# Optimization experiments

Hardware: AMD Instinct MI355X
Metric: run time of the kernel (lower is better)

Reference implementation:

```python
import jax, jax.numpy as jnp
import numpy as np

DIM = 768  # N, feature length and Linear dim
B, C = 16, 1024  # batch, token count


def setup_inputs() -> dict:
    key = jax.random.key(0)
    ks = jax.random.split(key, 7)
    s = 1.0 / np.sqrt(DIM)
    return {
        "x": jax.random.normal(ks[0], (B, C, DIM), dtype=jnp.float32),
        "Wq": jax.random.uniform(ks[1], (DIM, DIM), jnp.float32, -s, s),
        "bq": jax.random.uniform(ks[2], (DIM,), jnp.float32, -s, s),
        "Wk": jax.random.uniform(ks[3], (DIM, DIM), jnp.float32, -s, s),
        "bk": jax.random.uniform(ks[4], (DIM,), jnp.float32, -s, s),
        "Wv": jax.random.uniform(ks[5], (DIM, DIM), jnp.float32, -s, s),
        "bv": jax.random.uniform(ks[6], (DIM,), jnp.float32, -s, s),
    }


def reference(x, Wq, bq, Wk, bk, Wv, bv):
    # x: [B, C, N] with N == DIM; Linears act on last axis (torch y = x W^T + b)
    Bb, Cc, N = x.shape
    q = jnp.einsum("bcn,dn->bcd", x, Wq) + bq
    k = jnp.einsum("bcn,dn->bcd", x, Wk) + bk
    v = jnp.einsum("bcn,dn->bcd", x, Wv) + bv
    attn = jax.nn.softmax(jnp.einsum("bcd,bed->bce", q, k) * (N ** -0.5), axis=-1)  # [B,C,C]
    out = jnp.einsum("bce,ben->bcn", attn, v)  # [B,C,N]
    # faithful to torch: transpose(1,2) then reshape back to (B,C,N) -- a buffer reinterpretation
    out = jnp.transpose(out, (0, 2, 1)).reshape(Bb, Cc, N)
    return out + x  # dropout is identity at inference
```

## Files before the change

### kernel.cpp

```cpp
#include <hip/hip_runtime.h>
#include <hip/hip_bf16.h>

typedef __bf16 v8bf __attribute__((ext_vector_type(8)));
typedef float f32x4 __attribute__((ext_vector_type(4)));

static __device__ __forceinline__ unsigned short f2b(float f){
  union { float f; unsigned int u; } c; c.f = f;
  return (unsigned short)((c.u + 0x7FFFu + ((c.u >> 16) & 1u)) >> 16);
}
static __device__ __forceinline__ float b2f(unsigned int h){
  union { unsigned int u; float f; } c; c.u = h << 16; return c.f;
}

static __device__ __forceinline__ void gld_lds16(const void* g, void* l){
  __builtin_amdgcn_global_load_lds(
      (const __attribute__((address_space(1))) unsigned int*)g,
      (__attribute__((address_space(3))) unsigned int*)l, 16, 0, 0);
}

#define FENCE __builtin_amdgcn_sched_barrier(0)

static __device__ __forceinline__ void gemm128(
    const unsigned short* __restrict__ A, int lda,
    const unsigned short* __restrict__ B, int ldb,
    int NT, unsigned short* smem, f32x4 acc[4][3])
{
  const int tid  = threadIdx.x;
  const int lane = tid & 63;
  const int w    = tid >> 6;
  const int wr   = w >> 2, wc = w & 3;
  const int lr   = lane & 15, lg = lane >> 4;
  char* sm = (char*)smem;

  #pragma unroll
  for (int m=0;m<4;++m)
    #pragma unroll
    for (int n=0;n<3;++n)
      acc[m][n] = (f32x4){0.f,0.f,0.f,0.f};

  const int rloc = tid >> 3;
  const int scol = ((tid & 7) ^ ((tid >> 3) & 7)) << 3;
  const unsigned short* Ab0 = A + (size_t)rloc*lda + scol;
  const unsigned short* Bb0 = B + (size_t)rloc*ldb + scol;

  auto stA = [&](int d, int i, int kE){
    gld_lds16(Ab0 + (size_t)(i*64)*lda + kE, sm + d*16384 + i*8192 + w*1024);
  };
  auto stB = [&](int d, int i, int kE){
    gld_lds16(Bb0 + (size_t)(i*64)*ldb + kE, sm + 32768 + d*24576 + i*8192 + w*1024);
  };

  const int ce0 = (((lg*8))      ^ ((lr&7)<<3)) * 2;
  const int ce1 = (((32 + lg*8)) ^ ((lr&7)<<3)) * 2;

  stA(0,0,0); stA(0,1,0);
  stB(0,0,0); stB(0,1,0); stB(0,2,0);
  asm volatile("s_waitcnt vmcnt(0)" ::: "memory");
  __builtin_amdgcn_s_barrier();

  for (int kt = 0; kt < NT; ++kt) {
    const int d  = kt & 1;
    const int kN = (kt+1 < NT ? kt+1 : NT-1)*64;
    stA(d^1,0,kN); stA(d^1,1,kN);
    stB(d^1,0,kN); stB(d^1,1,kN); stB(d^1,2,kN);
    v8bf a[4][2], b[3][2];
    char* Abase = sm + d*16384;
    char* Bbase = sm + 32768 + d*24576;
    #pragma unroll
    for (int m=0;m<4;++m){
      char* rp = Abase + (wr*64 + m*16 + lr)*128;
      a[m][0] = *(const v8bf*)(rp + ce0);
      a[m][1] = *(const v8bf*)(rp + ce1);
    }
    #pragma unroll
    for (int n=0;n<3;++n){
      char* rp = Bbase + (wc*48 + n*16 + lr)*128;
      b[n][0] = *(const v8bf*)(rp + ce0);
      b[n][1] = *(const v8bf*)(rp + ce1);
    }
    FENCE; asm volatile("s_waitcnt lgkmcnt(0)" ::: "memory"); FENCE;
    __builtin_amdgcn_s_setprio(1);
    #pragma unroll
    for (int m=0;m<4;++m)
      #pragma unroll
      for (int n=0;n<3;++n){
        acc[m][n] = __builtin_amdgcn_mfma_f32_16x16x32_bf16(a[m][0], b[n][0], acc[m][n], 0,0,0);
        acc[m][n] = __builtin_amdgcn_mfma_f32_16x16x32_bf16(a[m][1], b[n][1], acc[m][n], 0,0,0);
      }
    __builtin_amdgcn_s_setprio(0);
    asm volatile("s_waitcnt vmcnt(0)" ::: "memory");
    __builtin_amdgcn_s_barrier();
  }
}

template<int NW, bool DEEP>
static __device__ __forceinline__ void gemmcore(
    const unsigned short* __restrict__ A, int lda,
    const unsigned short* __restrict__ B, int ldb,
    int NT, unsigned short* smem, f32x4 acc[8][NW])
{
  const int tid  = threadIdx.x;
  const int lane = tid & 63;
  const int w    = tid >> 6;
  const int wr   = w >> 2, wc = w & 3;
  const int lr   = lane & 15, lg = lane >> 4;
  char* sm = (char*)smem;
  constexpr int NAB   = DEEP ? 3 : 2;
  constexpr int BBASE = NAB * 32768;
  constexpr int BBUF  = NW * 8192;

  #pragma unroll
  for (int m=0;m<8;++m)
    #pragma unroll
    for (int n=0;n<NW;++n)
      acc[m][n] = (f32x4){0.f,0.f,0.f,0.f};

  const int rloc = tid >> 3;
  const int scol = ((tid & 7) ^ ((tid >> 3) & 7)) << 3;
  const unsigned short* Ab0 = A + (size_t)rloc*lda + scol;
  const unsigned short* Bb0 = B + (size_t)rloc*ldb + scol;

  auto stA = [&](int ab, int i, int kE){
    gld_lds16(Ab0 + (size_t)(i*64)*lda + kE, sm + ab*32768 + i*8192 + w*1024);
  };
  auto stB = [&](int db, int i, int kE){
    gld_lds16(Bb0 + (size_t)(i*64)*ldb + kE, sm + BBASE + db*BBUF + i*8192 + w*1024);
  };

  const int ce0 = (((lg*8))      ^ ((lr&7)<<3)) * 2;
  const int ce1 = (((32 + lg*8)) ^ ((lr&7)<<3)) * 2;

  v8bf bX[NW][2], bY[NW][2], af0[2][2], af1[2][2];

  auto rdA = [&](v8bf (&dst)[2][2], char* base, int qq){
    #pragma unroll
    for (int mm=0;mm<2;++mm){
      char* rp = base + ((qq*2+mm)*16+lr)*128;
      dst[mm][0] = *(const v8bf*)(rp + ce0);
      dst[mm][1] = *(const v8bf*)(rp + ce1);
    }
  };
  auto rdB = [&](v8bf (&dst)[NW][2], char* base){
    #pragma unroll
    for (int n=0;n<NW;++n){
      char* rp = base + (n*16+lr)*128;
      dst[n][0] = *(const v8bf*)(rp + ce0);
      dst[n][1] = *(const v8bf*)(rp + ce1);
    }
  };
  auto domfma = [&](v8bf (&a)[2][2], v8bf (&bb)[NW][2], int qq){
    __builtin_amdgcn_s_setprio(1);
    #pragma unroll
    for (int mm=0;mm<2;++mm)
      #pragma unroll
      for (int n=0;n<NW;++n){
        acc[qq*2+mm][n] = __builtin_amdgcn_mfma_f32_16x16x32_bf16(a[mm][0], bb[n][0], acc[qq*2+mm][n], 0,0,0);
        acc[qq*2+mm][n] = __builtin_amdgcn_mfma_f32_16x16x32_bf16(a[mm][1], bb[n][1], acc[qq*2+mm][n], 0,0,0);
      }
    __builtin_amdgcn_s_setprio(0);
  };

  auto ktile = [&](int kt, int ar, int an, int as,
                   v8bf (&bc)[NW][2], v8bf (&bn)[NW][2]){
    char* Ab = sm + ar*32768 + wr*16384;
    char* An = sm + an*32768 + wr*16384;
    char* Bn = sm + BBASE + ((kt+1)&1)*BBUF + wc*(NW*2048);
    const int kAraw = DEEP ? kt+2 : kt+1;
    const int kA = (kAraw < NT ? kAraw : NT-1)*64;
    const int kB = (kt+2 < NT ? kt+2 : NT-1)*64;
    const int db = kt & 1;

    stA(as,0,kA); stA(as,1,kA);
    rdA(af1, Ab, 1);
    FENCE; asm volatile("s_waitcnt lgkmcnt(4)" ::: "memory"); FENCE;
    domfma(af0, bc, 0);
    __builtin_amdgcn_s_barrier();

    stA(as,2,kA); stA(as,3,kA);
    rdA(af0, Ab, 2);
    FENCE; asm volatile("s_waitcnt lgkmcnt(4)" ::: "memory"); FENCE;
    domfma(af1, bc, 1);
    __builtin_amdgcn_s_barrier();

    stB(db,0,kB); stB(db,1,kB);
    rdA(af1, Ab, 3);
    FENCE; asm volatile("s_waitcnt lgkmcnt(4)" ::: "memory"); FENCE;
    domfma(af0, bc, 2);
    if constexpr (DEEP) asm volatile("s_waitcnt vmcnt(6)" ::: "memory");
    else                asm volatile("s_waitcnt vmcnt(2)" ::: "memory");
    __builtin_amdgcn_s_barrier();

    #pragma unroll
    for (int i=2;i<NW;++i) stB(db,i,kB);
    rdA(af0, An, 0);
    rdB(bn, Bn);
    if constexpr (NW==3) { FENCE; asm volatile("s_waitcnt lgkmcnt(10)" ::: "memory"); FENCE; }
    else                 { FENCE; asm volatile("s_waitcnt lgkmcnt(12)" ::: "memory"); FENCE; }
    domfma(af1, bc, 3);
    __builtin_amdgcn_s_barrier();
  };

  #pragma unroll
  for (int i=0;i<4;++i)  stA(0,i,0);
  #pragma unroll
  for (int i=0;i<NW;++i) stB(0,i,0);
  if constexpr (DEEP) {
    #pragma unroll
    for (int i=0;i<4;++i) stA(1,i,64);
  }
  #pragma unroll
  for (int i=0;i<NW;++i) stB(1,i,64);
  if constexpr (DEEP)      asm volatile("s_waitcnt vmcnt(7)" ::: "memory");
  else if constexpr (NW==3) asm volatile("s_waitcnt vmcnt(3)" ::: "memory");
  else                      asm volatile("s_waitcnt vmcnt(4)" ::: "memory");
  __builtin_amdgcn_s_barrier();
  rdB(bX, sm + BBASE + wc*(NW*2048));
  rdA(af0, sm + wr*16384, 0);

  if constexpr (DEEP) {
    int c0 = 0;
    for (int kt = 0; kt < NT; kt += 2) {
      const int c1 = (c0+1==3) ? 0 : c0+1;
      const int c2 = (c1+1==3) ? 0 : c1+1;
      ktile(kt,   c0, c1, c2, bX, bY);
      ktile(kt+1, c1, c2, c0, bY, bX);
      c0 = c2;
    }
  } else {
    for (int kt = 0; kt < NT; kt += 2) {
      ktile(kt,   0, 1, 1, bX, bY);
      ktile(kt+1, 1, 0, 0, bY, bX);
    }
  }
}

__global__ __launch_bounds__(256) void convert_kernel(
    const float* __restrict__ x,
    const float* __restrict__ Wq, const float* __restrict__ Wk,
    const float* __restrict__ Wv,
    unsigned short* __restrict__ Xb, unsigned short* __restrict__ Wb)
{
  const int NX = 3145728;
  const int NW_ = 147456;
  const int total = NX + 3*NW_;
  for (int i = blockIdx.x*256 + threadIdx.x; i < total; i += gridDim.x*256) {
    const float* src; unsigned short* dst; int off;
    if (i < NX) { src = x; dst = Xb; off = i; }
    else {
      int j = i - NX; int z = j / NW_; off = j - z*NW_;
      src = (z==0) ? Wq : ((z==1) ? Wk : Wv);
      dst = Wb + (size_t)z*589824;
    }
    float4 v = reinterpret_cast<const float4*>(src)[off];
    ushort4 h; h.x=f2b(v.x); h.y=f2b(v.y); h.z=f2b(v.z); h.w=f2b(v.w);
    reinterpret_cast<ushort4*>(dst)[off] = h;
  }
}

__global__ __launch_bounds__(512, 4) void qkv_kernel(
    const unsigned short* __restrict__ Xb, const unsigned short* __restrict__ Wb,
    const float* __restrict__ bq, const float* __restrict__ bk,
    const float* __restrict__ bv,
    unsigned short* __restrict__ Qb, unsigned short* __restrict__ Kb,
    unsigned short* __restrict__ Vt)
{
  extern __shared__ unsigned short smem[];
  const int bid = blockIdx.x;
  const int wg  = (bid & 7)*192 + (bid >> 3);
  const int mt  = wg / 12, nt = wg % 12;

  f32x4 acc[4][3];
  gemm128(Xb + (size_t)mt*128*768, 768,
          Wb + (size_t)nt*192*768, 768, 12, smem, acc);

  const int tid = threadIdx.x, lane = tid & 63, w = tid >> 6;
  const int wr = w >> 2, wc = w & 3, lr = lane & 15, lg = lane >> 4;
  const int z = nt >> 2;
  const float* bias = (z==0) ? bq : ((z==1) ? bk : bv);
  const int colbase = (nt & 3)*192 + wc*48;

  if (z < 2) {
    unsigned short* dst = (z==0) ? Qb : Kb;
    #pragma unroll
    for (int m=0;m<4;++m){
      int row0 = mt*128 + wr*64 + m*16 + lg*4;
      #pragma unroll
      for (int n=0;n<3;++n){
        int col = colbase + n*16 + lr;
        float bb = bias[col];
        #pragma unroll
        for (int r=0;r<4;++r)
          dst[(size_t)(row0+r)*768 + col] = f2b(acc[m][n][r] + bb);
      }
    }
  } else {
    const int batch = mt >> 3;
    const int ebase = (mt & 7)*128;
    unsigned short* dst = Vt + (size_t)batch*786432;
    #pragma unroll
    for (int m=0;m<4;++m){
      int e0 = ebase + wr*64 + m*16 + lg*4;
      #pragma unroll
      for (int n=0;n<3;++n){
        int col = colbase + n*16 + lr;
        float bb = bias[col];
        ushort4 h;
        h.x = f2b(acc[m][n][0] + bb);
        h.y = f2b(acc[m][n][1] + bb);
        h.z = f2b(acc[m][n][2] + bb);
        h.w = f2b(acc[m][n][3] + bb);
        *reinterpret_cast<ushort4*>(dst + (size_t)col*1024 + e0) = h;
      }
    }
  }
}

__global__ __launch_bounds__(512, 2) void scores_kernel(
    const unsigned short* __restrict__ Qb,
    const unsigned short* __restrict__ Kb,
    unsigned short* __restrict__ Eb)
{
  extern __shared__ unsigned short smem[];
  const int lid = blockIdx.x;
  const int seq = lid >> 3;
  const int b   = (lid & 7)*2 + (seq >> 4);
  const int t   = seq & 15;
  const int mt  = t >> 2, nt = t & 3;

  f32x4 acc[8][4];
  gemmcore<4,false>(Qb + (size_t)b*786432 + (size_t)mt*256*768, 768,
                    Kb + (size_t)b*786432 + (size_t)nt*256*768, 768,
                    12, smem, acc);

  const float scale = 0.03608439182435161f;
  const int tid = threadIdx.x, lane = tid & 63, w = tid >> 6;
  const int wr = w >> 2, wc = w & 3, lr = lane & 15, lg = lane >> 4;
  unsigned short* dst = Eb + (size_t)b*1048576;
  #pragma unroll
  for (int m=0;m<8;++m){
    int row0 = mt*256 + wr*128 + m*16 + lg*4;
    #pragma unroll
    for (int n=0;n<4;++n){
      int col = nt*256 + wc*64 + n*16 + lr;
      #pragma unroll
      for (int r=0;r<4;++r)
        dst[(size_t)(row0+r)*1024 + col] = f2b(__expf(acc[m][n][r] * scale));
    }
  }
}

__global__ __launch_bounds__(256) void rowsum_kernel(
    const unsigned short* __restrict__ E, float* __restrict__ D)
{
  int row  = blockIdx.x*4 + (threadIdx.x >> 6);
  int lane = threadIdx.x & 63;
  const unsigned short* p = E + (size_t)row*1024 + lane*16;
  uint4 v0 = *reinterpret_cast<const uint4*>(p);
  uint4 v1 = *reinterpret_cast<const uint4*>(p + 8);
  unsigned int uu[8] = {v0.x, v0.y, v0.z, v0.w, v1.x, v1.y, v1.z, v1.w};
  float s = 0.f;
  #pragma unroll
  for (int i=0;i<8;++i){ s += b2f(uu[i] & 0xffffu); s += b2f(uu[i] >> 16); }
  #pragma unroll
  for (int off=1; off<64; off<<=1) s += __shfl_xor(s, off, 64);
  if (lane == 0) D[row] = s;
}

__global__ __launch_bounds__(512, 2) void pv_kernel(
    const unsigned short* __restrict__ Eb,
    const unsigned short* __restrict__ Vt,
    const float* __restrict__ D,
    const float* __restrict__ x, float* __restrict__ out)
{
  extern __shared__ unsigned short smem[];
  const int lid = blockIdx.x;
  const int seq = lid >> 3;
  const int b   = (lid & 7)*2 + (seq >> 4);
  const int t   = seq & 15;
  const int mt  = t >> 2, nt = t & 3;

  f32x4 acc[8][3];
  gemmcore<3,true>(Eb + (size_t)b*1048576 + (size_t)mt*256*1024, 1024,
                   Vt + (size_t)b*786432  + (size_t)nt*192*1024, 1024,
                   16, smem, acc);

  const int tid = threadIdx.x, lane = tid & 63, w = tid >> 6;
  const int wr = w >> 2, wc = w & 3, lr = lane & 15, lg = lane >> 4;
  const float* xb = x   + (size_t)b*786432;
  float*       ob = out + (size_t)b*786432;
  const float* Db = D + b*1024;
  #pragma unroll
  for (int m=0;m<8;++m){
    int c0 = mt*256 + wr*128 + m*16 + lg*4;
    float inv0 = 1.0f / Db[c0+0];
    float inv1 = 1.0f / Db[c0+1];
    float inv2 = 1.0f / Db[c0+2];
    float inv3 = 1.0f / Db[c0+3];
    #pragma unroll
    for (int n=0;n<3;++n){
      int col = nt*192 + wc*48 + n*16 + lr;
      size_t idx = (size_t)col*1024 + c0;
      float4 xv = *reinterpret_cast<const float4*>(xb + idx);
      float4 o;
      o.x = acc[m][n][0]*inv0 + xv.x;
      o.y = acc[m][n][1]*inv1 + xv.y;
      o.z = acc[m][n][2]*inv2 + xv.z;
      o.w = acc[m][n][3]*inv3 + xv.w;
      *reinterpret_cast<float4*>(ob + idx) = o;
    }
  }
}

extern "C" void kernel_launch(void* const* d_in, const int* in_sizes, int n_in,
                              void* d_out, int out_size, void* d_ws, size_t ws_size,
                              hipStream_t stream)
{
  const float* x  = (const float*)d_in[0];
  const float* Wq = (const float*)d_in[1];
  const float* bq = (const float*)d_in[2];
  const float* Wk = (const float*)d_in[3];
  const float* bk = (const float*)d_in[4];
  const float* Wv = (const float*)d_in[5];
  const float* bv = (const float*)d_in[6];
  float* out = (float*)d_out;

  char* ws = (char*)d_ws;
  unsigned short* Xb = (unsigned short*)(ws);
  unsigned short* Wb = (unsigned short*)(ws + 25165824);
  unsigned short* Eb = (unsigned short*)(ws);
  unsigned short* Qb = (unsigned short*)(ws + 33554432);
  float*          Dd = (float*)         (ws + 33554432);
  unsigned short* Kb = (unsigned short*)(ws + 58720256);
  unsigned short* Vt = (unsigned short*)(ws + 83886080);

  convert_kernel<<<dim3(2048), dim3(256), 0,      stream>>>(x, Wq, Wk, Wv, Xb, Wb);
  qkv_kernel    <<<dim3(1536), dim3(512), 81920,  stream>>>(Xb, Wb, bq, bk, bv, Qb, Kb, Vt);
  scores_kernel <<<dim3(256),  dim3(512), 131072, stream>>>(Qb, Kb, Eb);
  rowsum_kernel <<<dim3(4096), dim3(256), 0,      stream>>>(Eb, Dd);
  pv_kernel     <<<dim3(256),  dim3(512), 147456, stream>>>(Eb, Vt, Dd, x, out);
}
```

Measured before the change: 144.4 us.

## Replace scores GEMM core with 8-phase, triple-buffered-B pipelined schedule

Adds a new GEMM core (gemm8p) for the QK^T scores kernel. It splits each K tile into four quadrant phases, interleaving global-to-LDS loads with MFMA work, and triple-buffers the B operand. The pv kernel keeps the old deep schedule, now specialised into gemmpv without templates. Scores LDS grows to 160KB, which could limit occupancy, and the extra barriers per phase add sync overhead.

```diff
diff --git a/kernel.cpp b/kernel.cpp
--- a/kernel.cpp
+++ b/kernel.cpp
@@ -19,6 +19,105 @@
 }
 
 #define FENCE __builtin_amdgcn_sched_barrier(0)
+
+static __device__ __forceinline__ void gemm8p(
+    const unsigned short* __restrict__ A, int lda,
+    const unsigned short* __restrict__ B, int ldb,
+    int NT, unsigned short* smem, f32x4 acc[8][4])
+{
+  const int tid  = threadIdx.x;
+  const int lane = tid & 63;
+  const int w    = tid >> 6;
+  const int wr   = w >> 2, wc = w & 3;
+  const int lr   = lane & 15, lg = lane >> 4;
+  char* sm = (char*)smem;
+
+  #pragma unroll
+  for (int m=0;m<8;++m)
+    #pragma unroll
+    for (int n=0;n<4;++n)
+      acc[m][n] = (f32x4){0.f,0.f,0.f,0.f};
+
+  const int rloc = tid >> 3;
+  const int scol = ((tid & 7) ^ ((tid >> 3) & 7)) << 3;
+  const unsigned short* Ab0 = A + (size_t)rloc*lda + scol;
+  const unsigned short* Bb0 = B + (size_t)rloc*ldb + scol;
+
+  auto stA2 = [&](int slot, int h, int kE){
+    gld_lds16(Ab0 + (size_t)(h*128)*lda + kE,      sm + slot*32768 + h*16384 + w*1024);
+    gld_lds16(Ab0 + (size_t)(h*128+64)*lda + kE,   sm + slot*32768 + h*16384 + 8192 + w*1024);
+  };
+  auto stB2 = [&](int slot, int h, int kE){
+    gld_lds16(Bb0 + (size_t)(h*128)*ldb + kE,      sm + 65536 + slot*32768 + h*16384 + w*1024);
+    gld_lds16(Bb0 + (size_t)(h*128+64)*ldb + kE,   sm + 65536 + slot*32768 + h*16384 + 8192 + w*1024);
+  };
+
+  const int ce0 = (((lg*8))      ^ ((lr&7)<<3)) * 2;
+  const int ce1 = (((32 + lg*8)) ^ ((lr&7)<<3)) * 2;
+
+  stA2(0,0,0); stA2(0,1,0);
+  stB2(0,0,0); stB2(0,1,0);
+  stB2(1,0,64); stB2(1,1,64);
+  asm volatile("s_waitcnt vmcnt(4)" ::: "memory");
+  __builtin_amdgcn_s_barrier();
+
+  int b0 = 0;
+  for (int kt = 0; kt < NT; kt += 2) {
+    const int b1 = (b0+1==3)?0:b0+1;
+    const int b2 = (b1+1==3)?0:b1+1;
+    const int kA1 = (kt+1 < NT ? kt+1 : NT-1)*64;
+    const int k2  = (kt+2 < NT ? kt+2 : NT-1)*64;
+    const int k3  = (kt+3 < NT ? kt+3 : NT-1)*64;
+
+    #pragma unroll
+    for (int tp=0; tp<2; ++tp) {
+      const int rdB = (tp==0) ? b0 : b1;
+      #pragma unroll
+      for (int q=0; q<4; ++q) {
+        const int mh = q>>1, nh = q&1;
+        v8bf a[4][2], b[2][2];
+        char* Ab = sm + tp*32768;
+        #pragma unroll
+        for (int mm=0;mm<4;++mm){
+          char* rp = Ab + (wr*128 + mh*64 + mm*16 + lr)*128;
+          a[mm][0] = *(const v8bf*)(rp + ce0);
+          a[mm][1] = *(const v8bf*)(rp + ce1);
+        }
+        char* Bb = sm + 65536 + rdB*32768;
+        #pragma unroll
+        for (int nn=0;nn<2;++nn){
+          char* rp = Bb + (wc*64 + nh*32 + nn*16 + lr)*128;
+          b[nn][0] = *(const v8bf*)(rp + ce0);
+          b[nn][1] = *(const v8bf*)(rp + ce1);
+        }
+        if      (tp==0 && q==0) stA2(1, 0, kA1);
+        else if (tp==0 && q==1) stA2(1, 1, kA1);
+        else if (tp==0 && q==2) stB2(b2, 0, k2);
+        else if (tp==0 && q==3) stB2(b2, 1, k2);
+        else if (tp==1 && q==0) stA2(0, 0, k2);
+        else if (tp==1 && q==1) stA2(0, 1, k2);
+        else if (tp==1 && q==2) stB2(b0, 0, k3);
+        else                    stB2(b0, 1, k3);
+
+        __builtin_amdgcn_s_barrier();
+        asm volatile("s_waitcnt lgkmcnt(0)" ::: "memory");
+        FENCE;
+        __builtin_amdgcn_s_setprio(1);
+        #pragma unroll
+        for (int mm=0;mm<4;++mm)
+          #pragma unroll
+          for (int nn=0;nn<2;++nn){
+            acc[mh*4+mm][nh*2+nn] = __builtin_amdgcn_mfma_f32_16x16x32_bf16(a[mm][0], b[nn][0], acc[mh*4+mm][nh*2+nn], 0,0,0);
+            acc[mh*4+mm][nh*2+nn] = __builtin_amdgcn_mfma_f32_16x16x32_bf16(a[mm][1], b[nn][1], acc[mh*4+mm][nh*2+nn], 0,0,0);
+          }
+        __builtin_amdgcn_s_setprio(0);
+        if (q==3) asm volatile("s_waitcnt vmcnt(4)" ::: "memory");
+        __builtin_amdgcn_s_barrier();
+      }
+    }
+    b0 = b2;
+  }
+}
 
 static __device__ __forceinline__ void gemm128(
     const unsigned short* __restrict__ A, int lda,
@@ -93,11 +192,10 @@
   }
 }
 
-template<int NW, bool DEEP>
-static __device__ __forceinline__ void gemmcore(
+static __device__ __forceinline__ void gemmpv(
     const unsigned short* __restrict__ A, int lda,
     const unsigned short* __restrict__ B, int ldb,
-    int NT, unsigned short* smem, f32x4 acc[8][NW])
+    int NT, unsigned short* smem, f32x4 acc[8][3])
 {
   const int tid  = threadIdx.x;
   const int lane = tid & 63;
@@ -105,14 +203,13 @@
   const int wr   = w >> 2, wc = w & 3;
   const int lr   = lane & 15, lg = lane >> 4;
   char* sm = (char*)smem;
-  constexpr int NAB   = DEEP ? 3 : 2;
-  constexpr int BBASE = NAB * 32768;
-  constexpr int BBUF  = NW * 8192;
+  constexpr int BBASE = 3 * 32768;
+  constexpr int BBUF  = 3 * 8192;
 
   #pragma unroll
   for (int m=0;m<8;++m)
     #pragma unroll
-    for (int n=0;n<NW;++n)
+    for (int n=0;n<3;++n)
       acc[m][n] = (f32x4){0.f,0.f,0.f,0.f};
 
   const int rloc = tid >> 3;
@@ -130,7 +227,7 @@
   const int ce0 = (((lg*8))      ^ ((lr&7)<<3)) * 2;
   const int ce1 = (((32 + lg*8)) ^ ((lr&7)<<3)) * 2;
 
-  v8bf bX[NW][2], bY[NW][2], af0[2][2], af1[2][2];
+  v8bf bX[3][2], bY[3][2], af0[2][2], af1[2][2];
 
   auto rdA = [&](v8bf (&dst)[2][2], char* base, int qq){
     #pragma unroll
@@ -140,20 +237,20 @@
       dst[mm][1] = *(const v8bf*)(rp + ce1);
     }
   };
-  auto rdB = [&](v8bf (&dst)[NW][2], char* base){
-    #pragma unroll
-    for (int n=0;n<NW;++n){
+  auto rdB = [&](v8bf (&dst)[3][2], char* base){
+    #pragma unroll
+    for (int n=0;n<3;++n){
       char* rp = base + (n*16+lr)*128;
       dst[n][0] = *(const v8bf*)(rp + ce0);
       dst[n][1] = *(const v8bf*)(rp + ce1);
     }
   };
-  auto domfma = [&](v8bf (&a)[2][2], v8bf (&bb)[NW][2], int qq){
+  auto domfma = [&](v8bf (&a)[2][2], v8bf (&bb)[3][2], int qq){
     __builtin_amdgcn_s_setprio(1);
     #pragma unroll
     for (int mm=0;mm<2;++mm)
       #pragma unroll
-      for (int n=0;n<NW;++n){
+      for (int n=0;n<3;++n){
         acc[qq*2+mm][n] = __builtin_amdgcn_mfma_f32_16x16x32_bf16(a[mm][0], bb[n][0], acc[qq*2+mm][n], 0,0,0);
         acc[qq*2+mm][n] = __builtin_amdgcn_mfma_f32_16x16x32_bf16(a[mm][1], bb[n][1], acc[qq*2+mm][n], 0,0,0);
       }
@@ -161,12 +258,11 @@
   };
 
   auto ktile = [&](int kt, int ar, int an, int as,
-                   v8bf (&bc)[NW][2], v8bf (&bn)[NW][2]){
+                   v8bf (&bc)[3][2], v8bf (&bn)[3][2]){
     char* Ab = sm + ar*32768 + wr*16384;
     char* An = sm + an*32768 + wr*16384;
-    char* Bn = sm + BBASE + ((kt+1)&1)*BBUF + wc*(NW*2048);
-    const int kAraw = DEEP ? kt+2 : kt+1;
-    const int kA = (kAraw < NT ? kAraw : NT-1)*64;
+    char* Bn = sm + BBASE + ((kt+1)&1)*BBUF + wc*(3*2048);
+    const int kA = (kt+2 < NT ? kt+2 : NT-1)*64;
     const int kB = (kt+2 < NT ? kt+2 : NT-1)*64;
     const int db = kt & 1;
 
@@ -186,51 +282,37 @@
     rdA(af1, Ab, 3);
     FENCE; asm volatile("s_waitcnt lgkmcnt(4)" ::: "memory"); FENCE;
     domfma(af0, bc, 2);
-    if constexpr (DEEP) asm volatile("s_waitcnt vmcnt(6)" ::: "memory");
-    else                asm volatile("s_waitcnt vmcnt(2)" ::: "memory");
+    asm volatile("s_waitcnt vmcnt(6)" ::: "memory");
     __builtin_amdgcn_s_barrier();
 
-    #pragma unroll
-    for (int i=2;i<NW;++i) stB(db,i,kB);
+    stB(db,2,kB);
     rdA(af0, An, 0);
     rdB(bn, Bn);
-    if constexpr (NW==3) { FENCE; asm volatile("s_waitcnt lgkmcnt(10)" ::: "memory"); FENCE; }
-    else                 { FENCE; asm volatile("s_waitcnt lgkmcnt(12)" ::: "memory"); FENCE; }
+    FENCE; asm volatile("s_waitcnt lgkmcnt(10)" ::: "memory"); FENCE;
     domfma(af1, bc, 3);
     __builtin_amdgcn_s_barrier();
   };
 
   #pragma unroll
-  for (int i=0;i<4;++i)  stA(0,i,0);
-  #pragma unroll
-  for (int i=0;i<NW;++i) stB(0,i,0);
-  if constexpr (DEEP) {
-    #pragma unroll
-    for (int i=0;i<4;++i) stA(1,i,64);
-  }
-  #pragma unroll
-  for (int i=0;i<NW;++i) stB(1,i,64);
-  if constexpr (DEEP)      asm volatile("s_waitcnt vmcnt(7)" ::: "memory");
-  else if constexpr (NW==3) asm volatile("s_waitcnt vmcnt(3)" ::: "memory");
-  else                      asm volatile("s_waitcnt vmcnt(4)" ::: "memory");
+  for (int i=0;i<4;++i) stA(0,i,0);
+  #pragma unroll
+  for (int i=0;i<3;++i) stB(0,i,0);
+  #pragma unroll
+  for (int i=0;i<4;++i) stA(1,i,64);
+  #pragma unroll
+  for (int i=0;i<3;++i) stB(1,i,64);
+  asm volatile("s_waitcnt vmcnt(7)" ::: "memory");
   __builtin_amdgcn_s_barrier();
-  rdB(bX, sm + BBASE + wc*(NW*2048));
+  rdB(bX, sm + BBASE + wc*(3*2048));
   rdA(af0, sm + wr*16384, 0);
 
-  if constexpr (DEEP) {
-    int c0 = 0;
-    for (int kt = 0; kt < NT; kt += 2) {
-      const int c1 = (c0+1==3) ? 0 : c0+1;
-      const int c2 = (c1+1==3) ? 0 : c1+1;
-      ktile(kt,   c0, c1, c2, bX, bY);
-      ktile(kt+1, c1, c2, c0, bY, bX);
-      c0 = c2;
-    }
-  } else {
-    for (int kt = 0; kt < NT; kt += 2) {
-      ktile(kt,   0, 1, 1, bX, bY);
-      ktile(kt+1, 1, 0, 0, bY, bX);
-    }
+  int c0 = 0;
+  for (int kt = 0; kt < NT; kt += 2) {
+    const int c1 = (c0+1==3) ? 0 : c0+1;
+    const int c2 = (c1+1==3) ? 0 : c1+1;
+    ktile(kt,   c0, c1, c2, bX, bY);
+    ktile(kt+1, c1, c2, c0, bY, bX);
+    c0 = c2;
   }
 }
 
@@ -328,9 +410,9 @@
   const int mt  = t >> 2, nt = t & 3;
 
   f32x4 acc[8][4];
-  gemmcore<4,false>(Qb + (size_t)b*786432 + (size_t)mt*256*768, 768,
-                    Kb + (size_t)b*786432 + (size_t)nt*256*768, 768,
-                    12, smem, acc);
+  gemm8p(Qb + (size_t)b*786432 + (size_t)mt*256*768, 768,
+         Kb + (size_t)b*786432 + (size_t)nt*256*768, 768,
+         12, smem, acc);
 
   const float scale = 0.03608439182435161f;
   const int tid = threadIdx.x, lane = tid & 63, w = tid >> 6;
@@ -380,9 +462,9 @@
   const int mt  = t >> 2, nt = t & 3;
 
   f32x4 acc[8][3];
-  gemmcore<3,true>(Eb + (size_t)b*1048576 + (size_t)mt*256*1024, 1024,
-                   Vt + (size_t)b*786432  + (size_t)nt*192*1024, 1024,
-                   16, smem, acc);
+  gemmpv(Eb + (size_t)b*1048576 + (size_t)mt*256*1024, 1024,
+         Vt + (size_t)b*786432  + (size_t)nt*192*1024, 1024,
+         16, smem, acc);
 
   const int tid = threadIdx.x, lane = tid & 63, w = tid >> 6;
   const int wr = w >> 2, wc = w & 3, lr = lane & 15, lg = lane >> 4;
@@ -435,7 +517,7 @@
 
   convert_kernel<<<dim3(2048), dim3(256), 0,      stream>>>(x, Wq, Wk, Wv, Xb, Wb);
   qkv_kernel    <<<dim3(1536), dim3(512), 81920,  stream>>>(Xb, Wb, bq, bk, bv, Qb, Kb, Vt);
-  scores_kernel <<<dim3(256),  dim3(512), 131072, stream>>>(Qb, Kb, Eb);
+  scores_kernel <<<dim3(256),  dim3(512), 163840, stream>>>(Qb, Kb, Eb);
   rowsum_kernel <<<dim3(4096), dim3(256), 0,      stream>>>(Eb, Dd);
   pv_kernel     <<<dim3(256),  dim3(512), 147456, stream>>>(Eb, Vt, Dd, x, out);
 }
```

New measurement: 147.6 us. +2.2%, slower.
